# Kernel tuning notes

Measured on AMD Instinct MI355X. Metric: run time of the kernel, lower is better.

Reference implementation:

```python
import jax, jax.numpy as jnp
import numpy as np

B, C, N, L, K, PRED = 64, 2, 1024, 24, 3, 12


def setup_inputs() -> dict:
    key = jax.random.key(0)
    ks = jax.random.split(key, 32)
    u = lambda k, shape, s: jax.random.uniform(k, shape, jnp.float32, -s, s)
    stdv_gc = 1.0 / np.sqrt(N)
    stdv_g = 1.0 / np.sqrt(N * (K + 1))
    stdv_r = 1.0 / np.sqrt(2 * N)
    inp = {
        'inputs': jax.random.normal(ks[0], (B, C, N, L), jnp.float32),
        'adj': (jax.random.uniform(ks[1], (N, N)) < 0.05).astype(jnp.float32),
        'gc_w': u(ks[2], (K, N, N), stdv_gc),
        'Wf': u(ks[3], (N, N * (K + 1)), stdv_g), 'bf': u(ks[4], (N,), stdv_g),
        'Wi': u(ks[5], (N, N * (K + 1)), stdv_g), 'bi': u(ks[6], (N,), stdv_g),
        'Wo': u(ks[7], (N, N * (K + 1)), stdv_g), 'bo': u(ks[8], (N,), stdv_g),
        'Wc': u(ks[9], (N, N * (K + 1)), stdv_g), 'bc': u(ks[10], (N,), stdv_g),
        'rWf': u(ks[11], (N, 2 * N), stdv_r), 'rbf': u(ks[12], (N,), stdv_r),
        'rWi': u(ks[13], (N, 2 * N), stdv_r), 'rbi': u(ks[14], (N,), stdv_r),
        'rWo': u(ks[15], (N, 2 * N), stdv_r), 'rbo': u(ks[16], (N,), stdv_r),
        'rWc': u(ks[17], (N, 2 * N), stdv_r), 'rbc': u(ks[18], (N,), stdv_r),
        'neighbor_w': u(ks[19], (N,), stdv_gc),
        'c': jnp.ones((1,), jnp.float32),
        'conv_w': u(ks[20], (C * PRED, C), 1.0 / np.sqrt(C)),
        'conv_b': u(ks[21], (C * PRED,), 1.0 / np.sqrt(C)),
    }
    return inp


def _build_A_list(adj, k):
    # tmp = sum(A, 0); zeros -> 1e-5; 'D_inverse' = diag(tmp) (as in original code)
    tmp = jnp.sum(adj, 0)
    tmp = jnp.where(tmp == 0, 1e-5, tmp)
    a_norm = tmp[:, None] * adj  # diag(tmp) @ A
    a_list = []
    a_tmp = jnp.eye(adj.shape[0], dtype=adj.dtype)
    for _ in range(k):
        a_tmp = jnp.minimum(a_tmp @ a_norm, 1.0)  # clamp max=1.0
        a_list.append(a_tmp)
    return a_list


def _forward(adj, inputs, gc_w, Wf, bf, Wi, bi, Wo, bo, Wc, bc,
             rWf, rbf, rWi, rbi, rWo, rbo, rWc, rbc, neighbor_w, c, conv_w, conv_b):
    b, ch, n, l = inputs.shape
    k = gc_w.shape[0]
    a_list = _build_A_list(adj, k)
    a_stack = jnp.stack(a_list)            # (K,N,N)
    eff_w = a_stack * gc_w                 # masked FilterLinear weights
    nbr = a_list[-1] @ neighbor_w          # (N,)
    Wg = jnp.concatenate([Wf, Wi, Wo, Wc], 0)      # fused gate weights (4N, (K+1)N)
    bg = jnp.concatenate([bf, bi, bo, bc], 0)
    rWg = jnp.concatenate([rWf, rWi, rWo, rWc], 0)  # (4N, 2N)
    rbg = jnp.concatenate([rbf, rbi, rbo, rbc], 0)

    def step(carry, x):  # x: (B,C,N)
        H, Cs, rH, rCs, _ = carry
        # gc = cat_k FilterLinear_k(x), each x @ (A_k*W_k)^T
        gc = jnp.einsum('bcn,kmn->bckm', x, eff_w).reshape(b, ch, k * n)
        g = jnp.concatenate([gc, H], -1) @ Wg.T + bg
        f, i, o, Ct = jnp.split(g, 4, -1)
        Cs = jax.nn.sigmoid(f) * (Cs * nbr) + jax.nn.sigmoid(i) * jnp.tanh(Ct)
        H = jax.nn.sigmoid(o) * jnp.tanh(Cs)
        rg = jnp.concatenate([x, rH], -1) @ rWg.T + rbg
        rf, ri, ro, rCt = jnp.split(rg, 4, -1)
        rCs = jax.nn.sigmoid(rf) * rCs + jax.nn.sigmoid(ri) * jnp.tanh(rCt)
        rH = jax.nn.sigmoid(ro) * jnp.tanh(rCs)
        var1 = jnp.var(x, axis=(0, 2), keepdims=True, ddof=1)   # (1,C,1), unbiased like torch
        var2 = jnp.var(gc, axis=(0, 2), keepdims=True, ddof=1)
        pred = (H * var1 * c + rH * var2) / (var1 + var2 * c)
        return (H, Cs, rH, rCs, pred), None

    z = jnp.zeros((b, ch, n), inputs.dtype)
    xs = jnp.moveaxis(inputs, -1, 0)  # (L,B,C,N)
    (H, Cs, rH, rCs, pred), _ = jax.lax.scan(step, (z, z, z, z, z), xs)
    # Conv1d(C, C*pred_len, k=1) then reshape (B,C,N,pred_len)
    out = jnp.einsum('bcn,oc->bon', pred, conv_w) + conv_b[:, None]
    return out.reshape(b, ch, n, -1)


def reference(inputs, adj, gc_w, Wf, bf, Wi, bi, Wo, bo, Wc, bc,
              rWf, rbf, rWi, rbi, rWo, rbo, rWc, rbc, neighbor_w, c, conv_w, conv_b):
    return _forward(adj, inputs, gc_w, Wf, bf, Wi, bi, Wo, bo, Wc, bc,
                    rWf, rbf, rWi, rbi, rWo, rbo, rWc, rbc, neighbor_w, c, conv_w, conv_b)
```

## Files before the change

kernel.cpp:

```cpp
#include <hip/hip_runtime.h>
#include <cmath>

#define NN 1024
#define BC 128
#define LS 24

typedef unsigned short u16;
typedef __attribute__((ext_vector_type(4))) float f32x4;
typedef __attribute__((ext_vector_type(8))) short bf16x8;

typedef __attribute__((address_space(1))) const void* as1cv;
typedef __attribute__((address_space(3))) void* as3v;

#define GLD16(gp, lp) __builtin_amdgcn_global_load_lds((as1cv)(gp), (as3v)(lp), 16, 0, 0)

__device__ __forceinline__ float sigf(float x){ return 1.0f/(1.0f+expf(-x)); }

__device__ __forceinline__ u16 f2b(float x){
  union { float f; unsigned u; } v; v.f = x;
  unsigned r = v.u + 0x7FFFu + ((v.u >> 16) & 1u);
  return (u16)(r >> 16);
}
__device__ __forceinline__ float b2f(u16 b){
  union { unsigned u; float f; } v; v.u = ((unsigned)b) << 16;
  return v.f;
}

__global__ void k_prep(const float* __restrict__ inputs, const float* __restrict__ adj,
                       const float* __restrict__ Wf, const float* __restrict__ Wi,
                       const float* __restrict__ Wo, const float* __restrict__ Wc,
                       const float* __restrict__ rWf, const float* __restrict__ rWi,
                       const float* __restrict__ rWo, const float* __restrict__ rWc,
                       const float* __restrict__ bf_, const float* __restrict__ bi_,
                       const float* __restrict__ bo_, const float* __restrict__ bc_,
                       const float* __restrict__ rbf, const float* __restrict__ rbi,
                       const float* __restrict__ rbo, const float* __restrict__ rbc,
                       u16* __restrict__ Xb, float* __restrict__ csum,
                       u16* __restrict__ Wgxb, u16* __restrict__ WgHp,
                       u16* __restrict__ rWgxb, u16* __restrict__ rWgHp,
                       float* __restrict__ bgcat){
  int b = blockIdx.x, tid = threadIdx.x;
  if (b < 512){
    int idx = b*256 + tid;
    const float4* p = (const float4*)(inputs + (size_t)idx*LS);
    float v[LS];
    #pragma unroll
    for (int q = 0; q < 6; ++q){
      float4 f = p[q];
      v[q*4]=f.x; v[q*4+1]=f.y; v[q*4+2]=f.z; v[q*4+3]=f.w;
    }
    #pragma unroll
    for (int t = 0; t < LS; ++t)
      Xb[(size_t)t*BC*NN + idx] = f2b(v[t]);
  } else if (b < 576){
    int bb = b - 512;
    for (int j = tid; j < 1024; j += 256){
      float s = 0.f;
      for (int i = 0; i < 16; ++i) s += adj[(size_t)(bb*16+i)*1024 + j];
      csum[(size_t)bb*1024 + j] = s;
    }
  } else if (b < 592){
    int idx = (b-576)*256 + tid;
    int seg = idx >> 10, j = idx & 1023;
    bgcat[idx]      = (seg==0?bf_: seg==1?bi_: seg==2?bo_:bc_)[j];
    bgcat[4096+idx] = (seg==0?rbf: seg==1?rbi: seg==2?rbo:rbc)[j];
  } else {
    int idx = (b-592)*256 + tid;
    if (idx < 16777216){
      int k = idx & 4095, r = idx >> 12, seg = r >> 10, j = r & 1023;
      const float* W = seg==0?Wf: seg==1?Wi: seg==2?Wo:Wc;
      float v = W[(size_t)j*4096 + k];
      if (k < 3072) Wgxb[(size_t)r*3072 + k] = f2b(v);
      else {
        int p = (j>>2)*16 + seg*4 + (j&3);
        WgHp[(size_t)p*1024 + (k-3072)] = f2b(v);
      }
    } else {
      int i2 = idx - 16777216;
      int k = i2 & 2047, r = i2 >> 11, seg = r >> 10, j = r & 1023;
      const float* W = seg==0?rWf: seg==1?rWi: seg==2?rWo:rWc;
      float v = W[(size_t)j*2048 + k];
      if (k < 1024) rWgxb[(size_t)r*1024 + k] = f2b(v);
      else {
        int p = (j>>2)*16 + seg*4 + (j&3);
        rWgHp[(size_t)p*1024 + (k-1024)] = f2b(v);
      }
    }
  }
}

__global__ void k_colsum2(const float* __restrict__ part, float* __restrict__ tmp){
  int j = blockIdx.x*256 + threadIdx.x;
  float s = 0.f;
  for (int b = 0; b < 64; ++b) s += part[(size_t)b*1024 + j];
  tmp[j] = (s == 0.f) ? 1e-5f : s;
}

__global__ void k_anormT(const float* __restrict__ adj, const float* __restrict__ tmp,
                         u16* __restrict__ A1b, u16* __restrict__ anormT){
  __shared__ u16 t[64][65];
  int bi = blockIdx.y*64, bj = blockIdx.x*64;
  for (int e = threadIdx.x; e < 4096; e += 256){
    int r = e >> 6, cc = e & 63;
    float v = tmp[bi+r]*adj[(size_t)(bi+r)*1024 + bj+cc];
    A1b[(size_t)(bi+r)*1024 + bj+cc] = f2b(fminf(v, 1.f));
    t[r][cc] = f2b(v);
  }
  __syncthreads();
  for (int e = threadIdx.x; e < 4096; e += 256){
    int r = e >> 6, cc = e & 63;
    anormT[(size_t)(bj+r)*1024 + bi+cc] = t[cc][r];
  }
}

__global__ void k_nbr(const u16* __restrict__ A3b, const float* __restrict__ nw,
                      float* __restrict__ nbr){
  __shared__ float red[256];
  int row = blockIdx.x;
  float s = 0.f;
  for (int j = threadIdx.x; j < 1024; j += 256)
    s += b2f(A3b[(size_t)row*1024 + j])*nw[j];
  red[threadIdx.x] = s; __syncthreads();
  for (int st = 128; st > 0; st >>= 1){
    if (threadIdx.x < st) red[threadIdx.x] += red[threadIdx.x+st];
    __syncthreads();
  }
  if (threadIdx.x == 0) nbr[row] = red[0];
}

__global__ void k_effT(const u16* __restrict__ Ap, const float* __restrict__ gcw,
                       u16* __restrict__ effb, u16* __restrict__ effbT){
  __shared__ u16 t[64][65];
  int bi = blockIdx.y*64, bj = blockIdx.x*64;
  for (int e = threadIdx.x; e < 4096; e += 256){
    int r = e >> 6, cc = e & 63;
    size_t idx = (size_t)(bi+r)*1024 + bj+cc;
    u16 v = f2b(b2f(Ap[idx]) * gcw[idx]);
    effb[idx] = v;
    t[r][cc] = v;
  }
  __syncthreads();
  for (int e = threadIdx.x; e < 4096; e += 256){
    int r = e >> 6, cc = e & 63;
    effbT[(size_t)(bj+r)*3072 + bi+cc] = t[cc][r];
  }
}

__device__ __forceinline__ void stage128(const u16* __restrict__ A, const u16* __restrict__ B,
                                         int K, int k0, u16* lA, u16* lB, int w, int lane){
  const int lrow = lane >> 3;
  const int srck = ((lane & 7) ^ lrow) * 8;
  #pragma unroll
  for (int c = 0; c < 4; ++c){
    int row = w*32 + c*8;
    GLD16(A + (size_t)(row + lrow)*K + k0 + srck, &lA[row*64]);
    GLD16(B + (size_t)(row + lrow)*K + k0 + srck, &lB[row*64]);
  }
}

__device__ __forceinline__ void mfma_tile(
    const u16* __restrict__ A, const u16* __restrict__ Bw, int K,
    const float* __restrict__ bias,
    float* __restrict__ outf, u16* __restrict__ outb, int ldc)
{
  __shared__ u16 ldsA[128*64];
  __shared__ u16 ldsB[128*64];
  const int tid  = threadIdx.x;
  const int lane = tid & 63;
  const int w    = tid >> 6;
  const int wr   = (w >> 1) * 64;
  const int wc   = (w & 1) * 64;
  f32x4 acc[4][4] = {};

  for (int k0 = 0; k0 < K; k0 += 64){
    stage128(A, Bw, K, k0, ldsA, ldsB, w, lane);
    __syncthreads();
    #pragma unroll
    for (int kk = 0; kk < 2; ++kk) {
      bf16x8 af[4], bfr[4];
      #pragma unroll
      for (int mi = 0; mi < 4; ++mi) {
        int row = wr + mi*16 + (lane & 15);
        int grp = (kk*4 + (lane >> 4)) ^ (row & 7);
        af[mi] = *(const bf16x8*)&ldsA[row*64 + grp*8];
      }
      #pragma unroll
      for (int ni = 0; ni < 4; ++ni) {
        int row = wc + ni*16 + (lane & 15);
        int grp = (kk*4 + (lane >> 4)) ^ (row & 7);
        bfr[ni] = *(const bf16x8*)&ldsB[row*64 + grp*8];
      }
      #pragma unroll
      for (int mi = 0; mi < 4; ++mi)
        #pragma unroll
        for (int ni = 0; ni < 4; ++ni)
          acc[mi][ni] = __builtin_amdgcn_mfma_f32_16x16x32_bf16(af[mi], bfr[ni], acc[mi][ni], 0, 0, 0);
    }
    __syncthreads();
  }
  #pragma unroll
  for (int mi = 0; mi < 4; ++mi) {
    #pragma unroll
    for (int ni = 0; ni < 4; ++ni) {
      int col = wc + ni*16 + (lane & 15);
      #pragma unroll
      for (int q = 0; q < 4; ++q) {
        int row = wr + mi*16 + (lane >> 4)*4 + q;
        float v = acc[mi][ni][q];
        if (bias) v += bias[col];
        if (outf) outf[(size_t)row*ldc + col] = v;
        if (outb) outb[(size_t)row*ldc + col] = f2b(v);
      }
    }
  }
}

__global__ __launch_bounds__(256) void k_mfma_nt(
    const u16* __restrict__ A, const u16* __restrict__ B, int K,
    const float* __restrict__ bias, float* __restrict__ outf,
    u16* __restrict__ outb, int ldc)
{
  size_t i0 = (size_t)blockIdx.y * 128, j0 = (size_t)blockIdx.x * 128;
  mfma_tile(A + i0*K, B + j0*K, K,
            bias ? bias + j0 : nullptr,
            outf ? outf + i0*ldc + j0 : nullptr,
            outb ? outb + i0*ldc + j0 : nullptr, ldc);
}

__global__ __launch_bounds__(256) void k_mfma64(
    const u16* __restrict__ Ag, const u16* __restrict__ Bg, int K,
    int clamp1, u16* __restrict__ outb, int ldc)
{
  __shared__ u16 ldsA[64*128];
  __shared__ u16 ldsB[64*128];
  const int tid  = threadIdx.x;
  const int lane = tid & 63;
  const int w    = tid >> 6;
  const int wr   = (w >> 1) * 32;
  const int wc   = (w & 1) * 32;
  const u16* A = Ag + (size_t)blockIdx.y*64*K;
  const u16* B = Bg + (size_t)blockIdx.x*64*K;
  f32x4 acc[2][2] = {};

  const int r4  = lane >> 4;
  const int g16 = lane & 15;
  for (int k0 = 0; k0 < K; k0 += 128){
    #pragma unroll
    for (int c = 0; c < 4; ++c){
      int rowb = w*16 + c*4;
      int row = rowb + r4;
      int srcg = (g16 & 8) | ((g16 & 7) ^ (row & 7));
      GLD16(A + (size_t)row*K + k0 + srcg*8, &ldsA[rowb*128]);
      GLD16(B + (size_t)row*K + k0 + srcg*8, &ldsB[rowb*128]);
    }
    __syncthreads();
    #pragma unroll
    for (int kk = 0; kk < 4; ++kk){
      int idx = kk*4 + (lane >> 4);
      bf16x8 af[2], bfr[2];
      #pragma unroll
      for (int mi = 0; mi < 2; ++mi){
        int row = wr + mi*16 + (lane & 15);
        int pa = (idx & 8) | ((idx & 7) ^ (row & 7));
        af[mi] = *(const bf16x8*)&ldsA[row*128 + pa*8];
      }
      #pragma unroll
      for (int ni = 0; ni < 2; ++ni){
        int row = wc + ni*16 + (lane & 15);
        int pb = (idx & 8) | ((idx & 7) ^ (row & 7));
        bfr[ni] = *(const bf16x8*)&ldsB[row*128 + pb*8];
      }
      #pragma unroll
      for (int mi = 0; mi < 2; ++mi)
        #pragma unroll
        for (int ni = 0; ni < 2; ++ni)
          acc[mi][ni] = __builtin_amdgcn_mfma_f32_16x16x32_bf16(af[mi], bfr[ni], acc[mi][ni], 0, 0, 0);
    }
    __syncthreads();
  }
  #pragma unroll
  for (int mi = 0; mi < 2; ++mi){
    #pragma unroll
    for (int ni = 0; ni < 2; ++ni){
      int col = blockIdx.x*64 + wc + ni*16 + (lane & 15);
      #pragma unroll
      for (int q = 0; q < 4; ++q){
        int row = blockIdx.y*64 + wr + mi*16 + (lane >> 4)*4 + q;
        float v = acc[mi][ni][q];
        if (clamp1) v = fminf(v, 1.f);
        outb[(size_t)row*ldc + col] = f2b(v);
      }
    }
  }
}

__global__ __launch_bounds__(256) void k_step(
    const u16* __restrict__ WgHp, const u16* __restrict__ rWgHp,
    const u16* __restrict__ pre_t,
    const float* __restrict__ nbrv,
    u16* __restrict__ Hb2, u16* __restrict__ rHb2,
    float* __restrict__ Cs, float* __restrict__ rCs,
    float* __restrict__ Hf, float* __restrict__ rHf,
    int ph, int last)
{
  __shared__ u16 ldsA[64*256];
  __shared__ u16 ldsB[16*256];

  const int tid  = threadIdx.x;
  const int lane = tid & 63;
  const int w    = tid >> 6;
  const int bid  = blockIdx.x;
  const int job  = bid >> 9;
  const int rem  = bid & 511;
  const int s    = rem >> 1;
  const int r0   = (rem & 1) * 64;

  const u16* Bp   = (job ? rWgHp : WgHp) + (size_t)s*16*1024;
  const u16* Ab   = (job ? rHb2 : Hb2) + (size_t)ph*BC*NN + (size_t)r0*NN;
  const u16* pret = pre_t + (size_t)job*4096;
  u16* Hnext  = (job ? rHb2 : Hb2) + (size_t)(ph^1)*BC*NN;
  float* Csb  = job ? rCs : Cs;
  float* Hfin = job ? rHf : Hf;

  const int g32   = lane & 31;
  const int rhalf = lane >> 5;

  f32x4 acc = {};
  for (int t = 0; t < 4; ++t){
    int k0 = t*256;
    #pragma unroll
    for (int c = 0; c < 8; ++c){
      int rowb = w*16 + c*2;
      int row = rowb + rhalf;
      int srcg = (g32 & 24) | ((g32 & 7) ^ (row & 7));
      GLD16(Ab + (size_t)row*1024 + k0 + srcg*8, &ldsA[rowb*256]);
    }
    #pragma unroll
    for (int c = 0; c < 2; ++c){
      int rowb = w*4 + c*2;
      int row = rowb + rhalf;
      int srcg = (g32 & 24) | ((g32 & 7) ^ (row & 7));
      GLD16(Bp + (size_t)row*1024 + k0 + srcg*8, &ldsB[rowb*256]);
    }
    __syncthreads();
    #pragma unroll
    for (int kk = 0; kk < 8; ++kk){
      int idx = kk*4 + (lane >> 4);
      int rowa = w*16 + (lane & 15);
      int pa = (idx & 24) | ((idx & 7) ^ (rowa & 7));
      bf16x8 af = *(const bf16x8*)&ldsA[rowa*256 + pa*8];
      int rowb2 = lane & 15;
      int pb = (idx & 24) | ((idx & 7) ^ (rowb2 & 7));
      bf16x8 bv = *(const bf16x8*)&ldsB[rowb2*256 + pb*8];
      acc = __builtin_amdgcn_mfma_f32_16x16x32_bf16(af, bv, acc, 0, 0, 0);
    }
    __syncthreads();
  }

  const int pcol = lane & 15;
  const int gcol = (pcol >> 2)*1024 + s*4 + (pcol & 3);
  const bool act = (lane & 12) == 0;
  const int  col = s*4 + (lane & 3);
  float fac = 1.f;
  if (!job && act) fac = nbrv[col];
  #pragma unroll
  for (int q = 0; q < 4; ++q){
    int row = r0 + w*16 + (lane >> 4)*4 + q;
    float a = acc[q] + b2f(pret[(size_t)row*8192 + gcol]);
    float vi  = __shfl_xor(a, 4);
    float vo  = __shfl_xor(a, 8);
    float vct = __shfl_xor(a, 12);
    if (act){
      float fg = sigf(a), ig = sigf(vi), og = sigf(vo), ct = tanhf(vct);
      size_t cidx = (size_t)row*NN + col;
      float cs = fg*Csb[cidx]*fac + ig*ct;
      Csb[cidx] = cs;
      float h = og*tanhf(cs);
      Hnext[cidx] = f2b(h);
      if (last) Hfin[cidx] = h;
    }
  }
}

__global__ void k_var1(const u16* __restrict__ Xl, const u16* __restrict__ gcl,
                       float* __restrict__ part){
  int ch = blockIdx.x & 1, seg = blockIdx.x >> 1;
  int tid = threadIdx.x;
  float s1=0.f,q1=0.f,s2=0.f,q2=0.f;
  for (int bb = 0; bb < 2; ++bb){
    int row = (seg*2+bb)*2 + ch;
    const u16* xr = Xl + (size_t)row*1024;
    for (int n = tid; n < 1024; n += 256){ float v = b2f(xr[n]); s1 += v; q1 += v*v; }
    const u16* gr = gcl + (size_t)row*3072;
    for (int n = tid; n < 3072; n += 256){ float v = b2f(gr[n]); s2 += v; q2 += v*v; }
  }
  __shared__ float red[256][4];
  red[tid][0]=s1; red[tid][1]=q1; red[tid][2]=s2; red[tid][3]=q2;
  __syncthreads();
  for (int st = 128; st > 0; st >>= 1){
    if (tid < st){ for (int z = 0; z < 4; ++z) red[tid][z] += red[tid+st][z]; }
    __syncthreads();
  }
  if (tid == 0){ for (int z = 0; z < 4; ++z) part[(size_t)blockIdx.x*4 + z] = red[0][z]; }
}

__global__ void k_out(const float* __restrict__ H, const float* __restrict__ rH,
                      const float* __restrict__ part, const float* __restrict__ cptr,
                      const float* __restrict__ cw, const float* __restrict__ cb,
                      float* __restrict__ out){
  __shared__ float vsh[4];
  int tid = threadIdx.x;
  if (tid < 4){
    int ch = tid & 1, which = tid >> 1;
    float s = 0.f, q = 0.f;
    for (int seg = 0; seg < 32; ++seg){
      const float* p = part + (size_t)(seg*2+ch)*4 + which*2;
      s += p[0]; q += p[1];
    }
    float n = which ? 196608.f : 65536.f;
    vsh[tid] = (q - s*s/n) / (n - 1.f);
  }
  __syncthreads();
  int idx = blockIdx.x*256 + tid;
  int n = idx & 1023, b = idx >> 10;
  float c0 = cptr[0];
  float v10 = vsh[0], v11 = vsh[1], v20 = vsh[2], v21 = vsh[3];
  size_t i0 = (size_t)(b*2+0)*1024 + n, i1 = (size_t)(b*2+1)*1024 + n;
  float p0 = (H[i0]*v10*c0 + rH[i0]*v20) / (v10 + v20*c0);
  float p1 = (H[i1]*v11*c0 + rH[i1]*v21) / (v11 + v21*c0);
  float* ob = out + (size_t)b*24*1024 + n;
  #pragma unroll
  for (int o = 0; o < 24; ++o)
    ob[(size_t)o*1024] = p0*cw[o*2+0] + p1*cw[o*2+1] + cb[o];
}

extern "C" void kernel_launch(void* const* d_in, const int* in_sizes, int n_in,
                              void* d_out, int out_size, void* d_ws, size_t ws_size,
                              hipStream_t stream) {
  const float* inputs = (const float*)d_in[0];
  const float* adj    = (const float*)d_in[1];
  const float* gcw    = (const float*)d_in[2];
  const float* Wf  = (const float*)d_in[3];  const float* bf_ = (const float*)d_in[4];
  const float* Wi  = (const float*)d_in[5];  const float* bi_ = (const float*)d_in[6];
  const float* Wo  = (const float*)d_in[7];  const float* bo_ = (const float*)d_in[8];
  const float* Wc  = (const float*)d_in[9];  const float* bc_ = (const float*)d_in[10];
  const float* rWf = (const float*)d_in[11]; const float* rbf = (const float*)d_in[12];
  const float* rWi = (const float*)d_in[13]; const float* rbi = (const float*)d_in[14];
  const float* rWo = (const float*)d_in[15]; const float* rbo = (const float*)d_in[16];
  const float* rWc = (const float*)d_in[17]; const float* rbc = (const float*)d_in[18];
  const float* nw     = (const float*)d_in[19];
  const float* cscal  = (const float*)d_in[20];
  const float* convw  = (const float*)d_in[21];
  const float* convb  = (const float*)d_in[22];
  float* out = (float*)d_out;

  char* cur = (char*)d_ws;
  auto alloc = [&](size_t bytes) -> void* {
    void* p = cur; cur += (bytes + 255) & ~(size_t)255; return p;
  };
  u16*   Xb     = (u16*)  alloc((size_t)LS*BC*NN*2);
  float* csum   = (float*)alloc((size_t)64*1024*4);
  float* tmpv   = (float*)alloc(1024*4);
  u16*   anormT = (u16*)  alloc((size_t)NN*NN*2);
  u16*   Apowb  = (u16*)  alloc((size_t)3*NN*NN*2);
  float* nbrv   = (float*)alloc(1024*4);
  u16*   effb   = (u16*)  alloc((size_t)3*NN*NN*2);
  u16*   effbT  = (u16*)  alloc((size_t)3*NN*NN*2);
  u16*   Wgxb   = (u16*)  alloc((size_t)4096*3072*2);
  u16*   WgHp   = (u16*)  alloc((size_t)4096*1024*2);
  u16*   rWgHp  = (u16*)  alloc((size_t)4096*1024*2);
  u16*   Bcat   = (u16*)  alloc((size_t)8192*1024*2);
  float* bgcat  = (float*)alloc(8192*4);
  u16*   gclb   = (u16*)  alloc((size_t)BC*3072*2);
  u16*   prebuf = (u16*)  alloc((size_t)3072*8192*2);
  char*  zbase  = cur;
  u16*   Hb2    = (u16*)  alloc((size_t)2*BC*NN*2);
  u16*   rHb2   = (u16*)  alloc((size_t)2*BC*NN*2);
  float* Cs     = (float*)alloc((size_t)BC*NN*4);
  float* rCs    = (float*)alloc((size_t)BC*NN*4);
  size_t zlen   = (size_t)(cur - zbase);
  float* Hfv    = (float*)alloc((size_t)BC*NN*4);
  float* rHfv   = (float*)alloc((size_t)BC*NN*4);
  float* part   = (float*)alloc(64*4*4);

  u16* A1b = Apowb;
  u16* A2b = Apowb + (size_t)NN*NN;
  u16* A3b = Apowb + (size_t)2*NN*NN;
  u16* Cwb   = Bcat;
  u16* rWgxb = Bcat + (size_t)4096*1024;

  k_prep<<<592 + (16777216+8388608)/256, 256, 0, stream>>>(
      inputs, adj, Wf, Wi, Wo, Wc, rWf, rWi, rWo, rWc,
      bf_, bi_, bo_, bc_, rbf, rbi, rbo, rbc,
      Xb, csum, Wgxb, WgHp, rWgxb, rWgHp, bgcat);
  k_colsum2<<<4, 256, 0, stream>>>(csum, tmpv);
  dim3 g16(16, 16);
  k_anormT<<<g16, 256, 0, stream>>>(adj, tmpv, A1b, anormT);
  k_mfma64<<<g16, 256, 0, stream>>>(A1b, anormT, 1024, 1, A2b, 1024);
  k_mfma64<<<g16, 256, 0, stream>>>(A2b, anormT, 1024, 1, A3b, 1024);
  k_nbr<<<NN, 256, 0, stream>>>(A3b, nw, nbrv);
  dim3 geff(16, 48);
  k_effT<<<geff, 256, 0, stream>>>(Apowb, gcw, effb, effbT);

  dim3 gcwg(16, 64);
  k_mfma64<<<gcwg, 256, 0, stream>>>(Wgxb, effbT, 3072, 0, Cwb, 1024);
  dim3 gpre(64, 24);
  k_mfma_nt<<<gpre, 256, 0, stream>>>(Xb, Bcat, 1024, bgcat, nullptr, prebuf, 8192);
  dim3 ggcl(48, 2);
  k_mfma64<<<ggcl, 256, 0, stream>>>(Xb + (size_t)(LS-1)*BC*NN, effb, 1024, 0, gclb, 3072);

  hipMemsetAsync(zbase, 0, zlen, stream);

  for (int t = 0; t < LS; ++t)
    k_step<<<1024, 256, 0, stream>>>(WgHp, rWgHp,
        prebuf + (size_t)t*BC*8192,
        nbrv, Hb2, rHb2, Cs, rCs, Hfv, rHfv, t & 1, t == LS-1);

  k_var1<<<64, 256, 0, stream>>>(Xb + (size_t)(LS-1)*BC*NN, gclb, part);
  k_out<<<(64*1024)/256, 256, 0, stream>>>(Hfv, rHfv, part, cscal, convw, convb, out);
}
```

Before: 617.6 us.

## Fuse next-step input projection into recurrent step kernel and widen gate tiles

The big up-front input-projection GEMM over all 24 timesteps is replaced by one launch for step 0, plus extra blocks inside each recurrent step kernel that compute the next step's projection alongside the recurrence. The recurrent weight layout is regrouped to 8 columns per gate, so each step block handles 8 hidden units with two MFMA accumulators. The step grid drops from 1024 to 512 recurrence blocks plus 64 projection blocks. The aim is to overlap the projection GEMM with the latency-bound recurrent steps and to cut shuffles, at the cost of a larger LDS footprint and uneven per-block work inside each launch.

New measurement: 1.087 ms. 76.0% more time.

```diff
diff --git a/kernel.cpp b/kernel.cpp
--- a/kernel.cpp
+++ b/kernel.cpp
@@ -72,7 +72,7 @@
       float v = W[(size_t)j*4096 + k];
       if (k < 3072) Wgxb[(size_t)r*3072 + k] = f2b(v);
       else {
-        int p = (j>>2)*16 + seg*4 + (j&3);
+        int p = (j>>3)*32 + seg*8 + (j&7);
         WgHp[(size_t)p*1024 + (k-3072)] = f2b(v);
       }
     } else {
@@ -82,7 +82,7 @@
       float v = W[(size_t)j*2048 + k];
       if (k < 1024) rWgxb[(size_t)r*1024 + k] = f2b(v);
       else {
-        int p = (j>>2)*16 + seg*4 + (j&3);
+        int p = (j>>3)*32 + seg*8 + (j&7);
         rWgHp[(size_t)p*1024 + (k-1024)] = f2b(v);
       }
     }
@@ -146,25 +146,12 @@
   }
 }
 
-__device__ __forceinline__ void stage128(const u16* __restrict__ A, const u16* __restrict__ B,
-                                         int K, int k0, u16* lA, u16* lB, int w, int lane){
-  const int lrow = lane >> 3;
-  const int srck = ((lane & 7) ^ lrow) * 8;
-  #pragma unroll
-  for (int c = 0; c < 4; ++c){
-    int row = w*32 + c*8;
-    GLD16(A + (size_t)(row + lrow)*K + k0 + srck, &lA[row*64]);
-    GLD16(B + (size_t)(row + lrow)*K + k0 + srck, &lB[row*64]);
-  }
-}
-
 __device__ __forceinline__ void mfma_tile(
     const u16* __restrict__ A, const u16* __restrict__ Bw, int K,
     const float* __restrict__ bias,
-    float* __restrict__ outf, u16* __restrict__ outb, int ldc)
+    float* __restrict__ outf, u16* __restrict__ outb, int ldc,
+    u16* ldsA, u16* ldsB)
 {
-  __shared__ u16 ldsA[128*64];
-  __shared__ u16 ldsB[128*64];
   const int tid  = threadIdx.x;
   const int lane = tid & 63;
   const int w    = tid >> 6;
@@ -172,8 +159,15 @@
   const int wc   = (w & 1) * 64;
   f32x4 acc[4][4] = {};
 
+  const int lrow = lane >> 3;
+  const int srck = ((lane & 7) ^ lrow) * 8;
   for (int k0 = 0; k0 < K; k0 += 64){
-    stage128(A, Bw, K, k0, ldsA, ldsB, w, lane);
+    #pragma unroll
+    for (int c = 0; c < 4; ++c){
+      int row = w*32 + c*8;
+      GLD16(A  + (size_t)(row + lrow)*K + k0 + srck, &ldsA[row*64]);
+      GLD16(Bw + (size_t)(row + lrow)*K + k0 + srck, &ldsB[row*64]);
+    }
     __syncthreads();
     #pragma unroll
     for (int kk = 0; kk < 2; ++kk) {
@@ -220,11 +214,13 @@
     const float* __restrict__ bias, float* __restrict__ outf,
     u16* __restrict__ outb, int ldc)
 {
+  __shared__ u16 lds[16384];
   size_t i0 = (size_t)blockIdx.y * 128, j0 = (size_t)blockIdx.x * 128;
   mfma_tile(A + i0*K, B + j0*K, K,
             bias ? bias + j0 : nullptr,
             outf ? outf + i0*ldc + j0 : nullptr,
-            outb ? outb + i0*ldc + j0 : nullptr, ldc);
+            outb ? outb + i0*ldc + j0 : nullptr, ldc,
+            lds, lds + 8192);
 }
 
 __global__ __launch_bounds__(256) void k_mfma64(
@@ -297,35 +293,48 @@
 __global__ __launch_bounds__(256) void k_step(
     const u16* __restrict__ WgHp, const u16* __restrict__ rWgHp,
     const u16* __restrict__ pre_t,
+    const u16* __restrict__ Xb_next, const u16* __restrict__ Bcat,
+    const float* __restrict__ bgcat, u16* __restrict__ pre_next, int do_pre,
     const float* __restrict__ nbrv,
     u16* __restrict__ Hb2, u16* __restrict__ rHb2,
     float* __restrict__ Cs, float* __restrict__ rCs,
     float* __restrict__ Hf, float* __restrict__ rHf,
     int ph, int last)
 {
-  __shared__ u16 ldsA[64*256];
-  __shared__ u16 ldsB[16*256];
+  __shared__ u16 lds[24576];
 
   const int tid  = threadIdx.x;
   const int lane = tid & 63;
   const int w    = tid >> 6;
   const int bid  = blockIdx.x;
-  const int job  = bid >> 9;
-  const int rem  = bid & 511;
+
+  if (bid >= 512){
+    if (!do_pre) return;
+    size_t j0 = (size_t)(bid - 512) * 128;
+    mfma_tile(Xb_next, Bcat + j0*1024, 1024, bgcat + j0,
+              nullptr, pre_next + j0, 8192, lds, lds + 8192);
+    return;
+  }
+
+  const int job  = bid >> 8;
+  const int rem  = bid & 255;
   const int s    = rem >> 1;
   const int r0   = (rem & 1) * 64;
 
-  const u16* Bp   = (job ? rWgHp : WgHp) + (size_t)s*16*1024;
+  const u16* Bp   = (job ? rWgHp : WgHp) + (size_t)s*32*1024;
   const u16* Ab   = (job ? rHb2 : Hb2) + (size_t)ph*BC*NN + (size_t)r0*NN;
   const u16* pret = pre_t + (size_t)job*4096;
   u16* Hnext  = (job ? rHb2 : Hb2) + (size_t)(ph^1)*BC*NN;
   float* Csb  = job ? rCs : Cs;
   float* Hfin = job ? rHf : Hf;
 
+  u16* ldsA = lds;
+  u16* ldsB = lds + 16384;
+
   const int g32   = lane & 31;
   const int rhalf = lane >> 5;
 
-  f32x4 acc = {};
+  f32x4 acc[2] = {};
   for (int t = 0; t < 4; ++t){
     int k0 = t*256;
     #pragma unroll
@@ -336,8 +345,8 @@
       GLD16(Ab + (size_t)row*1024 + k0 + srcg*8, &ldsA[rowb*256]);
     }
     #pragma unroll
-    for (int c = 0; c < 2; ++c){
-      int rowb = w*4 + c*2;
+    for (int c = 0; c < 4; ++c){
+      int rowb = w*8 + c*2;
       int row = rowb + rhalf;
       int srcg = (g32 & 24) | ((g32 & 7) ^ (row & 7));
       GLD16(Bp + (size_t)row*1024 + k0 + srcg*8, &ldsB[rowb*256]);
@@ -349,29 +358,40 @@
       int rowa = w*16 + (lane & 15);
       int pa = (idx & 24) | ((idx & 7) ^ (rowa & 7));
       bf16x8 af = *(const bf16x8*)&ldsA[rowa*256 + pa*8];
-      int rowb2 = lane & 15;
-      int pb = (idx & 24) | ((idx & 7) ^ (rowb2 & 7));
-      bf16x8 bv = *(const bf16x8*)&ldsB[rowb2*256 + pb*8];
-      acc = __builtin_amdgcn_mfma_f32_16x16x32_bf16(af, bv, acc, 0, 0, 0);
-    }
-    __syncthreads();
-  }
-
-  const int pcol = lane & 15;
-  const int gcol = (pcol >> 2)*1024 + s*4 + (pcol & 3);
-  const bool act = (lane & 12) == 0;
-  const int  col = s*4 + (lane & 3);
+      #pragma unroll
+      for (int ni = 0; ni < 2; ++ni){
+        int rowb2 = ni*16 + (lane & 15);
+        int pb = (idx & 24) | ((idx & 7) ^ (rowb2 & 7));
+        bf16x8 bv = *(const bf16x8*)&ldsB[rowb2*256 + pb*8];
+        acc[ni] = __builtin_amdgcn_mfma_f32_16x16x32_bf16(af, bv, acc[ni], 0, 0, 0);
+      }
+    }
+    __syncthreads();
+  }
+
+  #pragma unroll
+  for (int ni = 0; ni < 2; ++ni){
+    int pcol = ni*16 + (lane & 15);
+    int gcol = (pcol >> 3)*1024 + s*8 + (pcol & 7);
+    #pragma unroll
+    for (int q = 0; q < 4; ++q){
+      int row = r0 + w*16 + (lane >> 4)*4 + q;
+      acc[ni][q] += b2f(pret[(size_t)row*8192 + gcol]);
+    }
+  }
+  const bool act = (lane & 15) < 8;
+  const int  c   = lane & 7;
+  const int  col = s*8 + c;
   float fac = 1.f;
   if (!job && act) fac = nbrv[col];
   #pragma unroll
   for (int q = 0; q < 4; ++q){
-    int row = r0 + w*16 + (lane >> 4)*4 + q;
-    float a = acc[q] + b2f(pret[(size_t)row*8192 + gcol]);
-    float vi  = __shfl_xor(a, 4);
-    float vo  = __shfl_xor(a, 8);
-    float vct = __shfl_xor(a, 12);
+    float a0 = acc[0][q], a1 = acc[1][q];
+    float p1 = __shfl_xor(a0, 8);
+    float p3 = __shfl_xor(a1, 8);
     if (act){
-      float fg = sigf(a), ig = sigf(vi), og = sigf(vo), ct = tanhf(vct);
+      int row = r0 + w*16 + (lane >> 4)*4 + q;
+      float fg = sigf(a0), ig = sigf(p1), og = sigf(a1), ct = tanhf(p3);
       size_t cidx = (size_t)row*NN + col;
       float cs = fg*Csb[cidx]*fac + ig*ct;
       Csb[cidx] = cs;
@@ -504,17 +524,21 @@
 
   dim3 gcwg(16, 64);
   k_mfma64<<<gcwg, 256, 0, stream>>>(Wgxb, effbT, 3072, 0, Cwb, 1024);
-  dim3 gpre(64, 24);
-  k_mfma_nt<<<gpre, 256, 0, stream>>>(Xb, Bcat, 1024, bgcat, nullptr, prebuf, 8192);
+  dim3 gpre0(64, 1);
+  k_mfma_nt<<<gpre0, 256, 0, stream>>>(Xb, Bcat, 1024, bgcat, nullptr, prebuf, 8192);
   dim3 ggcl(48, 2);
   k_mfma64<<<ggcl, 256, 0, stream>>>(Xb + (size_t)(LS-1)*BC*NN, effb, 1024, 0, gclb, 3072);
 
   hipMemsetAsync(zbase, 0, zlen, stream);
 
-  for (int t = 0; t < LS; ++t)
-    k_step<<<1024, 256, 0, stream>>>(WgHp, rWgHp,
+  for (int t = 0; t < LS; ++t){
+    int tn = (t+1 < LS) ? t+1 : t;
+    k_step<<<576, 256, 0, stream>>>(WgHp, rWgHp,
         prebuf + (size_t)t*BC*8192,
+        Xb + (size_t)tn*BC*NN, Bcat, bgcat,
+        prebuf + (size_t)tn*BC*8192, (t+1 < LS) ? 1 : 0,
         nbrv, Hb2, rHb2, Cs, rCs, Hfv, rHfv, t & 1, t == LS-1);
+  }
 
   k_var1<<<64, 256, 0, stream>>>(Xb + (size_t)(LS-1)*BC*NN, gclb, part);
   k_out<<<(64*1024)/256, 256, 0, stream>>>(Hfv, rHfv, part, cscal, convw, convb, out);
```
